# Optimization experiments

Measured on AMD Instinct MI355X. Metric: run time of the kernel, lower is better.

Reference implementation:

```python
import jax, jax.numpy as jnp
import numpy as np

D_IN = 1024
D_OUT = 1024
SEQ = 4096


def setup_inputs() -> dict:
    key = jax.random.key(0)
    kx, kq, kk, kv = jax.random.split(key, 4)
    s = 1.0 / np.sqrt(D_IN)
    return {
        "x": jax.random.normal(kx, (SEQ, D_IN), dtype=jnp.float32),
        # torch Linear weights: shape [d_out, d_in], y = x @ W.T
        "Wq": jax.random.uniform(kq, (D_OUT, D_IN), jnp.float32, -s, s),
        "Wk": jax.random.uniform(kk, (D_OUT, D_IN), jnp.float32, -s, s),
        "Wv": jax.random.uniform(kv, (D_OUT, D_IN), jnp.float32, -s, s),
    }


def reference(x, Wq, Wk, Wv):
    # QKV projections (no bias)
    q = x @ Wq.T  # [N, d_out]
    k = x @ Wk.T
    v = x @ Wv.T
    scale = 1.0 / jnp.sqrt(jnp.asarray(k.shape[-1], x.dtype))
    att = jax.nn.softmax((q @ k.T) * scale, axis=-1)  # [N, N]
    return att @ v  # [N, d_out]
```

## Files before the change

kernel.cpp:

```cpp
#include <hip/hip_runtime.h>
#include <hip/hip_bf16.h>
#include <math.h>

typedef __attribute__((ext_vector_type(8))) short short8;
typedef __attribute__((ext_vector_type(4))) float floatx4;

static __device__ __forceinline__ unsigned short f2bf(float f) {
    union { float f; unsigned int u; } a; a.f = f;
    unsigned int u = a.u;
    return (unsigned short)((u + 0x7FFFu + ((u >> 16) & 1u)) >> 16);
}
static __device__ __forceinline__ float bf2f(unsigned short h) {
    union { unsigned int u; float f; } a; a.u = ((unsigned int)h) << 16;
    return a.f;
}

static __device__ __forceinline__ void cvt8(const float* __restrict__ src,
                                            unsigned short* __restrict__ dst, int i) {
    float4 v0 = *(const float4*)(src + i);
    float4 v1 = *(const float4*)(src + i + 4);
    ushort4 o0, o1;
    o0.x = f2bf(v0.x); o0.y = f2bf(v0.y); o0.z = f2bf(v0.z); o0.w = f2bf(v0.w);
    o1.x = f2bf(v1.x); o1.y = f2bf(v1.y); o1.z = f2bf(v1.z); o1.w = f2bf(v1.w);
    *(ushort4*)(dst + i) = o0;
    *(ushort4*)(dst + i + 4) = o1;
}

struct CV { const float* x; unsigned short* xb;
            const float* W[3]; unsigned short* Wb[3]; float* l; };
__global__ __launch_bounds__(256)
void cvt_all(CV a) {
    int b = blockIdx.x, t = threadIdx.x;
    if (b < 2048) {
        cvt8(a.x, a.xb, (b * 256 + t) * 8);
    } else if (b < 3584) {
        int z  = (b - 2048) >> 9;
        int bb = (b - 2048) & 511;
        cvt8(a.W[z], a.Wb[z], (bb * 256 + t) * 8);
    } else {
        float4 zz = {0.f, 0.f, 0.f, 0.f};
        #pragma unroll
        for (int c = 0; c < 4; c++)
            *(float4*)(a.l + t * 16 + c * 4) = zz;
    }
}

#define DSR(dst, base, OFF)                                                    \
    asm volatile("ds_read_b128 %0, %1 offset:%2"                               \
                 : "=v"(dst) : "v"(base), "n"(OFF))
#define LGKM(N) asm volatile("s_waitcnt lgkmcnt(" #N ")" ::: "memory")
#define SBAR()  asm volatile("s_barrier" ::: "memory")

typedef __attribute__((address_space(3))) char* lds3p;

__device__ __forceinline__ void gemm256_core(
    const unsigned short* __restrict__ A, const unsigned short* __restrict__ B,
    int lda, int k_begin, int bm, int bn,
    unsigned short* lds, floatx4 (&acc)[8][4])
{
    const int t    = threadIdx.x;
    const int wave = t >> 6;
    const int lane = t & 63;
    const int wrow = wave >> 2;
    const int wcol = wave & 3;
    const int lm   = lane & 15;
    const int ce8  = (((lane >> 4) ^ ((lm >> 1) & 3)) << 3);

    const int srow = t >> 2;
    const int gsh  = (((t & 3) ^ ((srow >> 1) & 3)) << 3);
    const unsigned short* srcA = A + (size_t)(bm + srow) * lda + k_begin + gsh;
    const unsigned short* srcB = B + (size_t)(bn + srow) * lda + k_begin + gsh;
    const size_t rstep = (size_t)128 * lda;
    char* ldsc = (char*)lds;
    const int w1k = wave << 10;

    lds3p lp3 = (lds3p)lds;
    lds3p va = lp3 + (((wrow << 7) + lm) * 64 + (ce8 << 1));
    lds3p vb = lp3 + (65536 + ((wcol << 6) + lm) * 64 + (ce8 << 1));

#define STAGE(kind, kh, tau) do {                                              \
        int taue_ = (tau) >= 16 ? (tau) - 2 : (tau);   \
        int ko_ = (taue_ << 6) + ((kh) << 5);                                  \
        unsigned lo_ = ((kind) << 16) + (((tau) & 1) << 15) + ((kh) << 14) + w1k; \
        const unsigned short* s_ = ((kind) ? srcB : srcA) + ko_;               \
        __builtin_amdgcn_global_load_lds(                                      \
            (const __attribute__((address_space(1))) void*)s_,                 \
            (__attribute__((address_space(3))) void*)(ldsc + lo_), 16, 0, 0);  \
        __builtin_amdgcn_global_load_lds(                                      \
            (const __attribute__((address_space(1))) void*)(s_ + rstep),       \
            (__attribute__((address_space(3))) void*)(ldsc + lo_ + 8192), 16, 0, 0); \
    } while (0)

#define MFMA4(R, AV)                                                           \
    do {                                                                       \
        acc[R][0] = __builtin_amdgcn_mfma_f32_16x16x32_bf16(AV, b4[0], acc[R][0], 0, 0, 0); \
        acc[R][1] = __builtin_amdgcn_mfma_f32_16x16x32_bf16(AV, b4[1], acc[R][1], 0, 0, 0); \
        acc[R][2] = __builtin_amdgcn_mfma_f32_16x16x32_bf16(AV, b4[2], acc[R][2], 0, 0, 0); \
        acc[R][3] = __builtin_amdgcn_mfma_f32_16x16x32_bf16(AV, b4[3], acc[R][3], 0, 0, 0); \
    } while (0)

    STAGE(1, 0, 0); STAGE(0, 0, 0); STAGE(1, 1, 0); STAGE(0, 1, 0);
    STAGE(1, 0, 1); STAGE(0, 0, 1); STAGE(1, 1, 1);
    asm volatile("s_waitcnt vmcnt(6)" ::: "memory");
    SBAR();

    short8 na[4], b4[4];
    for (int t2 = 0; t2 < 16; t2 += 2) {
        #pragma unroll
        for (int s = 0; s < 8; s++) {
            const int hi = s >> 2;
            const int s4 = s & 3;
            const int ks = s4 >> 1, ih = s4 & 1;
            const int tc = t2 + hi;
            constexpr int DB = 32768, KH = 16384, FR = 1024;
            const int PB = hi * DB + ks * KH;
            if (s4 == 0 || s4 == 2) {
                DSR(b4[0], vb, PB + 0 * FR);
                DSR(b4[1], vb, PB + 1 * FR);
                DSR(b4[2], vb, PB + 2 * FR);
                DSR(b4[3], vb, PB + 3 * FR);
            }
            DSR(na[0], va, PB + (ih * 4 + 0) * FR);
            DSR(na[1], va, PB + (ih * 4 + 1) * FR);
            DSR(na[2], va, PB + (ih * 4 + 2) * FR);
            DSR(na[3], va, PB + (ih * 4 + 3) * FR);
            if      (s4 == 0) STAGE(0, 1, tc + 1);
            else if (s4 == 1) STAGE(1, 0, tc + 2);
            else if (s4 == 2) STAGE(0, 0, tc + 2);
            else              STAGE(1, 1, tc + 2);
            __builtin_amdgcn_s_setprio(1);
            LGKM(3); __builtin_amdgcn_sched_barrier(0);
            MFMA4(ih * 4 + 0, na[0]);
            LGKM(2); __builtin_amdgcn_sched_barrier(0);
            MFMA4(ih * 4 + 1, na[1]);
            LGKM(1); __builtin_amdgcn_sched_barrier(0);
            MFMA4(ih * 4 + 2, na[2]);
            LGKM(0); __builtin_amdgcn_sched_barrier(0);
            MFMA4(ih * 4 + 3, na[3]);
            __builtin_amdgcn_s_setprio(0);
            if (s4 == 3) asm volatile("s_waitcnt vmcnt(6)" ::: "memory");
            SBAR();
        }
    }
#undef STAGE
#undef MFMA4
}

__device__ __forceinline__ void tile_store256(unsigned short* sm,
                                              floatx4 (&acc)[8][4], float scale, int trans,
                                              unsigned short* __restrict__ C, int ldc,
                                              int rbase, int cbase)
{
    const int t = threadIdx.x, wave = t >> 6, lane = t & 63;
    const int wrow = wave >> 2, wcol = wave & 3;
    const int lm = lane & 15, rq = ((lane >> 4) << 2);
    #pragma unroll
    for (int h = 0; h < 2; h++) {
        __syncthreads();
        if (!trans) {
            if (wrow == h) {
                #pragma unroll
                for (int i = 0; i < 8; i++)
                    #pragma unroll
                    for (int j = 0; j < 4; j++)
                        #pragma unroll
                        for (int r = 0; r < 4; r++)
                            sm[(i * 16 + rq + r) * 264 + wcol * 64 + j * 16 + lm] =
                                f2bf(acc[i][j][r] * scale);
            }
        } else {
            if ((wcol >> 1) == h) {
                #pragma unroll
                for (int i = 0; i < 8; i++)
                    #pragma unroll
                    for (int j = 0; j < 4; j++) {
                        ushort4 v;
                        v.x = f2bf(acc[i][j][0] * scale);
                        v.y = f2bf(acc[i][j][1] * scale);
                        v.z = f2bf(acc[i][j][2] * scale);
                        v.w = f2bf(acc[i][j][3] * scale);
                        *(ushort4*)&sm[((wcol & 1) * 64 + j * 16 + lm) * 264 +
                                       wrow * 128 + i * 16 + rq] = v;
                    }
            }
        }
        __syncthreads();
        #pragma unroll
        for (int p = 0; p < 4; p++) {
            int row = p * 32 + (t >> 4);
            int c0  = (t & 15) * 8;
            *(short8*)&C[(size_t)(rbase + h * 128 + row) * ldc + cbase + c0] =
                *(const short8*)&sm[row * 264 + c0];
            *(short8*)&C[(size_t)(rbase + h * 128 + row) * ldc + cbase + c0 + 128] =
                *(const short8*)&sm[row * 264 + c0 + 128];
        }
    }
}

struct P3 { const unsigned short* W[3]; unsigned short* O[3]; };
__global__ __launch_bounds__(512, 2)
void proj3(const unsigned short* __restrict__ xb, P3 a) {
    __shared__ __align__(16) unsigned short lds[65536];
    const int lid = blockIdx.x;
    const int xcd = lid & 7, rem = lid >> 3;
    const int z   = rem >> 3;
    const int idx = xcd * 8 + (rem & 7);
    const int by = idx >> 2, bx = idx & 3;
    const int bm = by * 256, bn = bx * 256;

    floatx4 acc[8][4];
    #pragma unroll
    for (int i = 0; i < 8; i++)
        #pragma unroll
        for (int j = 0; j < 4; j++) { floatx4 zz = {0.f,0.f,0.f,0.f}; acc[i][j] = zz; }

    gemm256_core(xb, a.W[z], 1024, 0, bm, bn, lds, acc);

    const int trans = (z == 2);
    const float scale = (z == 0) ? 0.03125f : 1.0f;
    tile_store256(lds, acc, scale, trans, a.O[z],
                  trans ? 4096 : 1024, trans ? bn : bm, trans ? bm : bn);
}

__global__ __launch_bounds__(512, 2)
void gemm_ps(const unsigned short* __restrict__ q, const unsigned short* __restrict__ k,
             unsigned short* __restrict__ Pm, float* __restrict__ l) {
    __shared__ __align__(16) unsigned short lds[65536];
    const int lid = blockIdx.x;
    const int xcd = lid & 7, r32 = lid >> 3;
    const int by = ((xcd >> 1) << 2) + (r32 & 3);
    const int bx = ((xcd & 1) << 3) + (r32 >> 2);
    const int bm = by * 256, bn = bx * 256;

    floatx4 acc[8][4];
    #pragma unroll
    for (int i = 0; i < 8; i++)
        #pragma unroll
        for (int j = 0; j < 4; j++) { floatx4 zz = {0.f,0.f,0.f,0.f}; acc[i][j] = zz; }

    gemm256_core(q, k, 1024, 0, bm, bn, lds, acc);

    const int lane = threadIdx.x & 63, wave = threadIdx.x >> 6;
    const int wrow = wave >> 2;
    const int lm = lane & 15, rq = ((lane >> 4) << 2);
    #pragma unroll
    for (int i = 0; i < 8; i++) {
        #pragma unroll
        for (int r = 0; r < 4; r++) {
            float rs = 0.f;
            #pragma unroll
            for (int j = 0; j < 4; j++) {
                float e = __expf(acc[i][j][r]);
                acc[i][j][r] = e;
                rs += e;
            }
            rs += __shfl_xor(rs, 1);
            rs += __shfl_xor(rs, 2);
            rs += __shfl_xor(rs, 4);
            rs += __shfl_xor(rs, 8);
            if (lm == 0) atomicAdd(l + bm + wrow * 128 + i * 16 + rq + r, rs);
        }
    }
    tile_store256(lds, acc, 1.0f, 0, Pm, 4096, bm, bn);
}

__global__ __launch_bounds__(512, 2)
void gemm_osplit(const unsigned short* __restrict__ Pm, const unsigned short* __restrict__ vT,
                 unsigned short* __restrict__ Opart) {
    __shared__ __align__(16) unsigned short lds[65536];
    const int lid = blockIdx.x;
    const int xcd = lid & 7, r32 = lid >> 3;
    const int z   = r32 & 3;
    const int idx = (r32 >> 2) * 8 + xcd;
    const int by = idx >> 2, bx = idx & 3;

    floatx4 acc[8][4];
    #pragma unroll
    for (int i = 0; i < 8; i++)
        #pragma unroll
        for (int j = 0; j < 4; j++) { floatx4 zz = {0.f,0.f,0.f,0.f}; acc[i][j] = zz; }

    gemm256_core(Pm, vT, 4096, z * 1024, by * 256, bx * 256, lds, acc);

    tile_store256(lds, acc, 1.0f, 0, Opart + (size_t)z * (4096 * 1024), 1024,
                  by * 256, bx * 256);
}

__global__ __launch_bounds__(256)
void reduce_scale(const unsigned short* __restrict__ Op, const float* __restrict__ l,
                  float* __restrict__ out) {
    int i = (blockIdx.x * 256 + threadIdx.x) * 4;
    ushort4 a = *(const ushort4*)(Op + i);
    ushort4 b = *(const ushort4*)(Op + 4194304 + i);
    ushort4 c = *(const ushort4*)(Op + 8388608 + i);
    ushort4 d = *(const ushort4*)(Op + 12582912 + i);
    float inv = 1.0f / l[i >> 10];
    float4 o;
    o.x = (bf2f(a.x) + bf2f(b.x) + bf2f(c.x) + bf2f(d.x)) * inv;
    o.y = (bf2f(a.y) + bf2f(b.y) + bf2f(c.y) + bf2f(d.y)) * inv;
    o.z = (bf2f(a.z) + bf2f(b.z) + bf2f(c.z) + bf2f(d.z)) * inv;
    o.w = (bf2f(a.w) + bf2f(b.w) + bf2f(c.w) + bf2f(d.w)) * inv;
    *(float4*)(out + i) = o;
}

extern "C" void kernel_launch(void* const* d_in, const int* in_sizes, int n_in,
                              void* d_out, int out_size, void* d_ws, size_t ws_size,
                              hipStream_t stream) {
    const float* x  = (const float*)d_in[0];
    const float* Wq = (const float*)d_in[1];
    const float* Wk = (const float*)d_in[2];
    const float* Wv = (const float*)d_in[3];
    float* out = (float*)d_out;

    char* ws = (char*)d_ws;
    const size_t MB = 1u << 20;
    unsigned short* vTb = (unsigned short*)(ws);
    unsigned short* xb  = (unsigned short*)(ws + 8 * MB);
    unsigned short* Wqb = (unsigned short*)(ws + 16 * MB);
    unsigned short* Wkb = (unsigned short*)(ws + 18 * MB);
    unsigned short* Wvb = (unsigned short*)(ws + 20 * MB);
    unsigned short* qb  = (unsigned short*)(ws + 22 * MB);
    unsigned short* kb  = (unsigned short*)(ws + 30 * MB);
    unsigned short* P   = (unsigned short*)(ws + 40 * MB);
    float*          l   = (float*)(ws + 72 * MB);
    unsigned short* Opart = (unsigned short*)(ws + 8 * MB);

    dim3 b256(256), b512(512);
    CV cv = {x, xb, {Wq, Wk, Wv}, {Wqb, Wkb, Wvb}, l};
    cvt_all<<<dim3(3585), b256, 0, stream>>>(cv);

    P3 p3 = {{Wqb, Wkb, Wvb}, {qb, kb, vTb}};
    proj3<<<dim3(192), b512, 0, stream>>>(xb, p3);

    gemm_ps<<<dim3(256), b512, 0, stream>>>(qb, kb, P, l);

    gemm_osplit<<<dim3(256), b512, 0, stream>>>(P, vTb, Opart);

    reduce_scale<<<dim3(4096), b256, 0, stream>>>(Opart, l, out);
}
```

Measured before the change: 195.9 us.

## Software-pipeline LDS fragment reads one sub-step ahead of MFMAs in GEMM mainloop

The A and B LDS fragment reads for the next sub-step are now issued right after each MFMA group of the current step, with the first set prefetched before the loop. This overlaps LDS latency with matrix-core work instead of stalling at the start of each step. The global-load wait moves to before the STAGE issue and is relaxed from vmcnt(6) to vmcnt(4). Reads that cross the barrier into the next buffer rely on correct vmcnt/lgkmcnt accounting, so any mistake there risks a hazard.

```diff
diff --git a/kernel.cpp b/kernel.cpp
--- a/kernel.cpp
+++ b/kernel.cpp
@@ -104,44 +104,62 @@
     asm volatile("s_waitcnt vmcnt(6)" ::: "memory");
     SBAR();
 
+    constexpr int DB = 32768, KH = 16384, FR = 1024;
     short8 na[4], b4[4];
+    DSR(na[0], va, 0 * FR);
+    DSR(na[1], va, 1 * FR);
+    DSR(na[2], va, 2 * FR);
+    DSR(b4[0], vb, 0 * FR);
+    DSR(b4[1], vb, 1 * FR);
+    DSR(b4[2], vb, 2 * FR);
+    DSR(b4[3], vb, 3 * FR);
+    DSR(na[3], va, 3 * FR);
+
     for (int t2 = 0; t2 < 16; t2 += 2) {
         #pragma unroll
         for (int s = 0; s < 8; s++) {
             const int hi = s >> 2;
             const int s4 = s & 3;
-            const int ks = s4 >> 1, ih = s4 & 1;
+            const int ih = s4 & 1;
             const int tc = t2 + hi;
-            constexpr int DB = 32768, KH = 16384, FR = 1024;
-            const int PB = hi * DB + ks * KH;
-            if (s4 == 0 || s4 == 2) {
-                DSR(b4[0], vb, PB + 0 * FR);
-                DSR(b4[1], vb, PB + 1 * FR);
-                DSR(b4[2], vb, PB + 2 * FR);
-                DSR(b4[3], vb, PB + 3 * FR);
-            }
-            DSR(na[0], va, PB + (ih * 4 + 0) * FR);
-            DSR(na[1], va, PB + (ih * 4 + 1) * FR);
-            DSR(na[2], va, PB + (ih * 4 + 2) * FR);
-            DSR(na[3], va, PB + (ih * 4 + 3) * FR);
+            const int odd = s4 & 1;
+            const int sn  = s + 1;
+            const int hin = (sn >> 2) & 1;
+            const int s4n = sn & 3;
+            const int ksn = s4n >> 1, ihn = s4n & 1;
+            const int PBn = hin * DB + ksn * KH;
+
+            if (s4 == 3) asm volatile("s_waitcnt vmcnt(4)" ::: "memory");
             if      (s4 == 0) STAGE(0, 1, tc + 1);
             else if (s4 == 1) STAGE(1, 0, tc + 2);
             else if (s4 == 2) STAGE(0, 0, tc + 2);
             else              STAGE(1, 1, tc + 2);
             __builtin_amdgcn_s_setprio(1);
-            LGKM(3); __builtin_amdgcn_sched_barrier(0);
+            if (odd) { LGKM(3); } else { LGKM(1); }
+            __builtin_amdgcn_sched_barrier(0);
             MFMA4(ih * 4 + 0, na[0]);
-            LGKM(2); __builtin_amdgcn_sched_barrier(0);
+            DSR(na[0], va, PBn + (ihn * 4 + 0) * FR);
+            if (odd) { LGKM(3); __builtin_amdgcn_sched_barrier(0); }
             MFMA4(ih * 4 + 1, na[1]);
-            LGKM(1); __builtin_amdgcn_sched_barrier(0);
+            DSR(na[1], va, PBn + (ihn * 4 + 1) * FR);
+            if (odd) { LGKM(3); __builtin_amdgcn_sched_barrier(0); }
             MFMA4(ih * 4 + 2, na[2]);
-            LGKM(0); __builtin_amdgcn_sched_barrier(0);
+            DSR(na[2], va, PBn + (ihn * 4 + 2) * FR);
+            LGKM(3);
+            __builtin_amdgcn_sched_barrier(0);
             MFMA4(ih * 4 + 3, na[3]);
+            if (odd) {
+                DSR(b4[0], vb, PBn + 0 * FR);
+                DSR(b4[1], vb, PBn + 1 * FR);
+                DSR(b4[2], vb, PBn + 2 * FR);
+                DSR(b4[3], vb, PBn + 3 * FR);
+            }
+            DSR(na[3], va, PBn + (ihn * 4 + 3) * FR);
             __builtin_amdgcn_s_setprio(0);
-            if (s4 == 3) asm volatile("s_waitcnt vmcnt(6)" ::: "memory");
             SBAR();
         }
     }
+    LGKM(0);
 #undef STAGE
 #undef MFMA4
 }
```

Result: no change. 196.8 us (+0.4%).

## Double-buffer LDS fragment registers to overlap ds_reads with MFMA phases

Applied to the files above, without the earlier changes.

Restructures the GEMM inner loop into a four-phase schedule with ping-pong register sets for A and B fragments. The next phase's LDS reads are issued before the current MFMA group, so each MFMA block waits only on data loaded earlier instead of stalling per fragment. This adds register pressure from the doubled fragment arrays and extra barriers per phase, and changes the waitcnt and barrier choreography, which could expose races or spills.

```diff
diff --git a/kernel.cpp b/kernel.cpp
--- a/kernel.cpp
+++ b/kernel.cpp
@@ -48,8 +48,12 @@
 #define DSR(dst, base, OFF)                                                    \
     asm volatile("ds_read_b128 %0, %1 offset:%2"                               \
                  : "=v"(dst) : "v"(base), "n"(OFF))
+#define DSR4(arr, base, O)                                                     \
+    do { DSR(arr[0], base, (O));        DSR(arr[1], base, (O) + 1024);         \
+         DSR(arr[2], base, (O) + 2048); DSR(arr[3], base, (O) + 3072); } while (0)
 #define LGKM(N) asm volatile("s_waitcnt lgkmcnt(" #N ")" ::: "memory")
 #define SBAR()  asm volatile("s_barrier" ::: "memory")
+#define SB0     __builtin_amdgcn_sched_barrier(0)
 
 typedef __attribute__((address_space(3))) char* lds3p;
 
@@ -91,59 +95,74 @@
             (__attribute__((address_space(3))) void*)(ldsc + lo_ + 8192), 16, 0, 0); \
     } while (0)
 
-#define MFMA4(R, AV)                                                           \
+#define MF1(R, AV, BV)                                                         \
     do {                                                                       \
-        acc[R][0] = __builtin_amdgcn_mfma_f32_16x16x32_bf16(AV, b4[0], acc[R][0], 0, 0, 0); \
-        acc[R][1] = __builtin_amdgcn_mfma_f32_16x16x32_bf16(AV, b4[1], acc[R][1], 0, 0, 0); \
-        acc[R][2] = __builtin_amdgcn_mfma_f32_16x16x32_bf16(AV, b4[2], acc[R][2], 0, 0, 0); \
-        acc[R][3] = __builtin_amdgcn_mfma_f32_16x16x32_bf16(AV, b4[3], acc[R][3], 0, 0, 0); \
+        acc[R][0] = __builtin_amdgcn_mfma_f32_16x16x32_bf16(AV, BV[0], acc[R][0], 0, 0, 0); \
+        acc[R][1] = __builtin_amdgcn_mfma_f32_16x16x32_bf16(AV, BV[1], acc[R][1], 0, 0, 0); \
+        acc[R][2] = __builtin_amdgcn_mfma_f32_16x16x32_bf16(AV, BV[2], acc[R][2], 0, 0, 0); \
+        acc[R][3] = __builtin_amdgcn_mfma_f32_16x16x32_bf16(AV, BV[3], acc[R][3], 0, 0, 0); \
     } while (0)
+#define MFMAG(R0, NA, BV)                                                      \
+    do { MF1((R0) + 0, NA[0], BV); MF1((R0) + 1, NA[1], BV);                   \
+         MF1((R0) + 2, NA[2], BV); MF1((R0) + 3, NA[3], BV); } while (0)
 
     STAGE(1, 0, 0); STAGE(0, 0, 0); STAGE(1, 1, 0); STAGE(0, 1, 0);
     STAGE(1, 0, 1); STAGE(0, 0, 1); STAGE(1, 1, 1);
     asm volatile("s_waitcnt vmcnt(6)" ::: "memory");
     SBAR();
 
-    short8 na[4], b4[4];
+    constexpr int DB = 32768, KH = 16384;
+    short8 naA[4], naB[4], bA[4], bB[4];
+    DSR4(naA, va, 0);
+    DSR4(bA,  vb, 0);
+
+#define FOURPH(PBc, PBn, TC)                                                   \
+                         \
+    DSR4(naB, va, (PBc) + 4096);                                               \
+    STAGE(0, 1, (TC) + 1);                                                     \
+    SBAR(); LGKM(4); SB0;                                                      \
+    __builtin_amdgcn_s_setprio(1);                                             \
+    MFMAG(0, naA, bA); SB0;                                                    \
+    __builtin_amdgcn_s_setprio(0);                                             \
+    SBAR();                                                                    \
+         \
+    DSR4(naA, va, (PBc) + KH);                                                 \
+    DSR4(bB,  vb, (PBc) + KH);                                                 \
+    STAGE(1, 0, (TC) + 2);                                                     \
+    SBAR(); LGKM(8); SB0;                                                      \
+    __builtin_amdgcn_s_setprio(1);                                             \
+    MFMAG(4, naB, bA); SB0;                                                    \
+    __builtin_amdgcn_s_setprio(0);                                             \
+    SBAR();                                                                    \
+                         \
+    DSR4(naB, va, (PBc) + KH + 4096);                                          \
+    STAGE(0, 0, (TC) + 2);                                                     \
+    SBAR(); LGKM(4); SB0;                                                      \
+    __builtin_amdgcn_s_setprio(1);                                             \
+    MFMAG(0, naA, bB); SB0;                                                    \
+    __builtin_amdgcn_s_setprio(0);                                             \
+    SBAR();                                                                    \
+     \
+    asm volatile("s_waitcnt vmcnt(4)" ::: "memory");                           \
+    STAGE(1, 1, (TC) + 2);                                                     \
+    SBAR();                                                                    \
+    DSR4(naA, va, (PBn));                                                      \
+    DSR4(bA,  vb, (PBn));                                                      \
+    LGKM(8); SB0;                                                              \
+    __builtin_amdgcn_s_setprio(1);                                             \
+    MFMAG(4, naB, bB); SB0;                                                    \
+    __builtin_amdgcn_s_setprio(0);                                             \
+    SBAR();
+
     for (int t2 = 0; t2 < 16; t2 += 2) {
-        #pragma unroll
-        for (int s = 0; s < 8; s++) {
-            const int hi = s >> 2;
-            const int s4 = s & 3;
-            const int ks = s4 >> 1, ih = s4 & 1;
-            const int tc = t2 + hi;
-            constexpr int DB = 32768, KH = 16384, FR = 1024;
-            const int PB = hi * DB + ks * KH;
-            if (s4 == 0 || s4 == 2) {
-                DSR(b4[0], vb, PB + 0 * FR);
-                DSR(b4[1], vb, PB + 1 * FR);
-                DSR(b4[2], vb, PB + 2 * FR);
-                DSR(b4[3], vb, PB + 3 * FR);
-            }
-            DSR(na[0], va, PB + (ih * 4 + 0) * FR);
-            DSR(na[1], va, PB + (ih * 4 + 1) * FR);
-            DSR(na[2], va, PB + (ih * 4 + 2) * FR);
-            DSR(na[3], va, PB + (ih * 4 + 3) * FR);
-            if      (s4 == 0) STAGE(0, 1, tc + 1);
-            else if (s4 == 1) STAGE(1, 0, tc + 2);
-            else if (s4 == 2) STAGE(0, 0, tc + 2);
-            else              STAGE(1, 1, tc + 2);
-            __builtin_amdgcn_s_setprio(1);
-            LGKM(3); __builtin_amdgcn_sched_barrier(0);
-            MFMA4(ih * 4 + 0, na[0]);
-            LGKM(2); __builtin_amdgcn_sched_barrier(0);
-            MFMA4(ih * 4 + 1, na[1]);
-            LGKM(1); __builtin_amdgcn_sched_barrier(0);
-            MFMA4(ih * 4 + 2, na[2]);
-            LGKM(0); __builtin_amdgcn_sched_barrier(0);
-            MFMA4(ih * 4 + 3, na[3]);
-            __builtin_amdgcn_s_setprio(0);
-            if (s4 == 3) asm volatile("s_waitcnt vmcnt(6)" ::: "memory");
-            SBAR();
-        }
+        FOURPH(0, DB, t2);
+        FOURPH(DB, 0, t2 + 1);
     }
+    LGKM(0);
+#undef FOURPH
 #undef STAGE
-#undef MFMA4
+#undef MFMAG
+#undef MF1
 }
 
 __device__ __forceinline__ void tile_store256(unsigned short* sm,
```

After: 197.0 us. No clear change (+0.6%).

## Restructure GEMM main loop into four barrier regions with two stages each

Applied to the files above, without the earlier changes.

Rewrites the 256x256 bf16 GEMM inner loop so that each region covers a full k-half and runs all eight A fragments against one B fragment load. Each region issues two global-to-LDS stage loads instead of one, and the barrier count per pair of tiles drops from eight to four. The vmcnt wait moves to the start of each region with a deeper outstanding count. The aim is to cut barrier and synchronisation overhead and keep more memory traffic in flight, at the cost of a changed prefetch schedule. That schedule could race or stall if the vmcnt accounting is wrong, and the STAGE calls past the last tile may now load beyond the tile range.

```diff
diff --git a/kernel.cpp b/kernel.cpp
--- a/kernel.cpp
+++ b/kernel.cpp
@@ -48,8 +48,12 @@
 #define DSR(dst, base, OFF)                                                    \
     asm volatile("ds_read_b128 %0, %1 offset:%2"                               \
                  : "=v"(dst) : "v"(base), "n"(OFF))
+#define DSR4(arr, base, O)                                                     \
+    do { DSR(arr[0], base, (O));        DSR(arr[1], base, (O) + 1024);         \
+         DSR(arr[2], base, (O) + 2048); DSR(arr[3], base, (O) + 3072); } while (0)
 #define LGKM(N) asm volatile("s_waitcnt lgkmcnt(" #N ")" ::: "memory")
 #define SBAR()  asm volatile("s_barrier" ::: "memory")
+#define SB0     __builtin_amdgcn_sched_barrier(0)
 
 typedef __attribute__((address_space(3))) char* lds3p;
 
@@ -99,49 +103,38 @@
         acc[R][3] = __builtin_amdgcn_mfma_f32_16x16x32_bf16(AV, b4[3], acc[R][3], 0, 0, 0); \
     } while (0)
 
-    STAGE(1, 0, 0); STAGE(0, 0, 0); STAGE(1, 1, 0); STAGE(0, 1, 0);
-    STAGE(1, 0, 1); STAGE(0, 0, 1); STAGE(1, 1, 1);
-    asm volatile("s_waitcnt vmcnt(6)" ::: "memory");
-    SBAR();
-
+    STAGE(0, 0, 0); STAGE(1, 0, 0); STAGE(0, 1, 0); STAGE(1, 1, 0);
+    STAGE(0, 0, 1); STAGE(1, 0, 1);
+
+    constexpr int DB = 32768, KH = 16384;
     short8 na[4], b4[4];
+
+#define REGION(PBc, KHO, k1, h1, t1, k2, h2, t2)                               \
+    asm volatile("s_waitcnt vmcnt(8)" ::: "memory");                           \
+    SBAR();                                                                    \
+    STAGE(k1, h1, t1); STAGE(k2, h2, t2);                                      \
+    __builtin_amdgcn_s_setprio(1);                                             \
+    DSR4(b4, vb, (PBc) + (KHO));                                               \
+    DSR4(na, va, (PBc) + (KHO));                                               \
+    LGKM(3); SB0; MFMA4(0, na[0]);                                             \
+    LGKM(2); SB0; MFMA4(1, na[1]);                                             \
+    LGKM(1); SB0; MFMA4(2, na[2]);                                             \
+    LGKM(0); SB0; MFMA4(3, na[3]);                                             \
+    DSR4(na, va, (PBc) + (KHO) + 4096);                                        \
+    LGKM(3); SB0; MFMA4(4, na[0]);                                             \
+    LGKM(2); SB0; MFMA4(5, na[1]);                                             \
+    LGKM(1); SB0; MFMA4(6, na[2]);                                             \
+    LGKM(0); SB0; MFMA4(7, na[3]);                                             \
+    __builtin_amdgcn_s_setprio(0);
+
     for (int t2 = 0; t2 < 16; t2 += 2) {
-        #pragma unroll
-        for (int s = 0; s < 8; s++) {
-            const int hi = s >> 2;
-            const int s4 = s & 3;
-            const int ks = s4 >> 1, ih = s4 & 1;
-            const int tc = t2 + hi;
-            constexpr int DB = 32768, KH = 16384, FR = 1024;
-            const int PB = hi * DB + ks * KH;
-            if (s4 == 0 || s4 == 2) {
-                DSR(b4[0], vb, PB + 0 * FR);
-                DSR(b4[1], vb, PB + 1 * FR);
-                DSR(b4[2], vb, PB + 2 * FR);
-                DSR(b4[3], vb, PB + 3 * FR);
-            }
-            DSR(na[0], va, PB + (ih * 4 + 0) * FR);
-            DSR(na[1], va, PB + (ih * 4 + 1) * FR);
-            DSR(na[2], va, PB + (ih * 4 + 2) * FR);
-            DSR(na[3], va, PB + (ih * 4 + 3) * FR);
-            if      (s4 == 0) STAGE(0, 1, tc + 1);
-            else if (s4 == 1) STAGE(1, 0, tc + 2);
-            else if (s4 == 2) STAGE(0, 0, tc + 2);
-            else              STAGE(1, 1, tc + 2);
-            __builtin_amdgcn_s_setprio(1);
-            LGKM(3); __builtin_amdgcn_sched_barrier(0);
-            MFMA4(ih * 4 + 0, na[0]);
-            LGKM(2); __builtin_amdgcn_sched_barrier(0);
-            MFMA4(ih * 4 + 1, na[1]);
-            LGKM(1); __builtin_amdgcn_sched_barrier(0);
-            MFMA4(ih * 4 + 2, na[2]);
-            LGKM(0); __builtin_amdgcn_sched_barrier(0);
-            MFMA4(ih * 4 + 3, na[3]);
-            __builtin_amdgcn_s_setprio(0);
-            if (s4 == 3) asm volatile("s_waitcnt vmcnt(6)" ::: "memory");
-            SBAR();
-        }
+        REGION(0,  0,  0, 1, t2 + 1, 1, 1, t2 + 1);
+        REGION(0,  KH, 0, 0, t2 + 2, 1, 0, t2 + 2);
+        REGION(DB, 0,  0, 1, t2 + 2, 1, 1, t2 + 2);
+        REGION(DB, KH, 0, 0, t2 + 3, 1, 0, t2 + 3);
     }
+    LGKM(0);
+#undef REGION
 #undef STAGE
 #undef MFMA4
 }
```

Result: slower. 200.7 us (+2.4%).
